# Kernel optimization log

Hardware: AMD Instinct MI355X
Metric: run time of the kernel (lower is better)

Reference implementation:

```python
import jax, jax.numpy as jnp
import numpy as np

B, C, H, W = 8, 3, 512, 512


def _spd(key, shape_prefix, c):
    a = jax.random.normal(key, shape_prefix + (c, c), dtype=jnp.float32)
    return a @ jnp.swapaxes(a, -1, -2) + jnp.eye(c, dtype=jnp.float32)


def setup_inputs() -> dict:
    key = jax.random.key(0)
    k1, k2, k3, k4, k5 = jax.random.split(key, 5)
    target = jax.random.normal(k1, (B, C, H, W), dtype=jnp.float32)
    mu = jax.random.normal(k2, (B, C, H, W), dtype=jnp.float32)
    # per-pixel covariance matrices; sigma_y must be SPD for inverse/log-det
    sigma_mu = _spd(k3, (B, H, W), C)
    sigma_n = _spd(k4, (B, H, W), C)
    sigma_y = _spd(k5, (B, H, W), C)
    return {"target": target, "mu": mu, "sigma_mu": sigma_mu,
            "sigma_n": sigma_n, "sigma_y": sigma_y}


def reference(target, mu, sigma_mu, sigma_n, sigma_y):
    # T: residual per pixel, channels-last  [B,H,W,C]
    T = jnp.transpose(target - mu, (0, 2, 3, 1))
    inv = jnp.linalg.inv(sigma_y)                      # [B,H,W,C,C] tiny 3x3 batched inverse
    # quadratic form 0.5 * T^t Sigma^{-1} T            [B,H,W]
    t1 = 0.5 * jnp.einsum('bhwc,bhwcd,bhwd->bhw', T, inv, T)
    t2 = 0.5 * jnp.log(jnp.linalg.det(sigma_y))        # [B,H,W]
    loss = jnp.mean(t1 + t2)
    # torch code zeroes loss if quadratic term blows up
    loss = jnp.where(jnp.max(t1) > 1e8, jnp.zeros_like(loss), loss)
    return loss
```

## Files before the change

### kernel.cpp

```cpp
#include <hip/hip_runtime.h>

constexpr int Cc = 3;
constexpr int Hc = 512;
constexpr int Wc = 512;
constexpr int HW = Hc * Wc;
constexpr int NPIX = 8 * HW;
constexpr int NGRP = NPIX / 4;
constexpr int NBLK = NGRP / 256;


__global__ __launch_bounds__(256) void map_loss_main(
    const float* __restrict__ target,
    const float* __restrict__ mu,
    const float* __restrict__ sigma_y,
    double* __restrict__ part_sum,
    float* __restrict__ part_max)
{
    double local_sum = 0.0;
    float local_max = 0.0f;

    int g = blockIdx.x * blockDim.x + threadIdx.x;
    {
        int p0 = g << 2;
        int b  = p0 >> 18;
        int hw = p0 & (HW - 1);
        long long base = (long long)b * (Cc * HW) + hw;

        const float4* tg = (const float4*)(target + base);
        const float4* mm = (const float4*)(mu + base);
        float4 d0 = tg[0];            float4 m0 = mm[0];
        float4 d1 = tg[HW / 4];       float4 m1 = mm[HW / 4];
        float4 d2 = tg[2 * HW / 4];   float4 m2 = mm[2 * HW / 4];
        d0.x -= m0.x; d0.y -= m0.y; d0.z -= m0.z; d0.w -= m0.w;
        d1.x -= m1.x; d1.y -= m1.y; d1.z -= m1.z; d1.w -= m1.w;
        d2.x -= m2.x; d2.y -= m2.y; d2.z -= m2.z; d2.w -= m2.w;

        union { float4 v[9]; float f[36]; } S;
        const float4* s4 = (const float4*)(sigma_y + (long long)p0 * 9);
        #pragma unroll
        for (int i = 0; i < 9; ++i) S.v[i] = s4[i];

        const float T0[4] = {d0.x, d0.y, d0.z, d0.w};
        const float T1[4] = {d1.x, d1.y, d1.z, d1.w};
        const float T2[4] = {d2.x, d2.y, d2.z, d2.w};

        #pragma unroll
        for (int i = 0; i < 4; ++i) {
            const float* s = S.f + i * 9;
            float s00 = s[0], s01 = s[1], s02 = s[2];
            float s11 = s[4], s12 = s[5], s22 = s[8];

            float a00 = s11 * s22 - s12 * s12;
            float a01 = s02 * s12 - s01 * s22;
            float a02 = s01 * s12 - s02 * s11;
            float a11 = s00 * s22 - s02 * s02;
            float a12 = s01 * s02 - s00 * s12;
            float a22 = s00 * s11 - s01 * s01;

            float det = s00 * a00 + s01 * a01 + s02 * a02;

            float t0 = T0[i], t1 = T1[i], t2 = T2[i];
            float quad = t0 * t0 * a00 + t1 * t1 * a11 + t2 * t2 * a22
                       + 2.0f * (t0 * t1 * a01 + t0 * t2 * a02 + t1 * t2 * a12);

            float t1term = 0.5f * quad / det;
            float t2term = 0.5f * logf(det);

            local_sum += (double)(t1term + t2term);
            local_max = fmaxf(local_max, t1term);
        }
    }

    for (int off = 32; off > 0; off >>= 1) {
        local_sum += __shfl_down(local_sum, off, 64);
        local_max = fmaxf(local_max, __shfl_down(local_max, off, 64));
    }

    __shared__ double ssum[4];
    __shared__ float  smax[4];
    int wave = threadIdx.x >> 6;
    int lane = threadIdx.x & 63;
    if (lane == 0) { ssum[wave] = local_sum; smax[wave] = local_max; }
    __syncthreads();

    if (threadIdx.x == 0) {
        part_sum[blockIdx.x] = ssum[0] + ssum[1] + ssum[2] + ssum[3];
        part_max[blockIdx.x] = fmaxf(fmaxf(smax[0], smax[1]), fmaxf(smax[2], smax[3]));
    }
}

__global__ __launch_bounds__(256) void map_loss_finalize(
    const double* __restrict__ part_sum,
    const float* __restrict__ part_max,
    float* __restrict__ out)
{
    double s = 0.0;
    float m = 0.0f;
    for (int i = threadIdx.x; i < NBLK; i += 256) {
        s += part_sum[i];
        m = fmaxf(m, part_max[i]);
    }

    for (int off = 32; off > 0; off >>= 1) {
        s += __shfl_down(s, off, 64);
        m = fmaxf(m, __shfl_down(m, off, 64));
    }

    __shared__ double ssum[4];
    __shared__ float  smax[4];
    int wave = threadIdx.x >> 6;
    int lane = threadIdx.x & 63;
    if (lane == 0) { ssum[wave] = s; smax[wave] = m; }
    __syncthreads();

    if (threadIdx.x == 0) {
        double bs = ssum[0] + ssum[1] + ssum[2] + ssum[3];
        float  bm = fmaxf(fmaxf(smax[0], smax[1]), fmaxf(smax[2], smax[3]));
        out[0] = (bm > 1e8f) ? 0.0f : (float)(bs / (double)NPIX);
    }
}

extern "C" void kernel_launch(void* const* d_in, const int* in_sizes, int n_in,
                              void* d_out, int out_size, void* d_ws, size_t ws_size,
                              hipStream_t stream) {
    const float* target  = (const float*)d_in[0];
    const float* mu      = (const float*)d_in[1];
    const float* sigma_y = (const float*)d_in[4];
    float* out = (float*)d_out;

    double* part_sum = (double*)d_ws;
    float*  part_max = (float*)((char*)d_ws + NBLK * sizeof(double));

    map_loss_main<<<NBLK, 256, 0, stream>>>(target, mu, sigma_y, part_sum, part_max);
    map_loss_finalize<<<1, 256, 0, stream>>>(part_sum, part_max, out);
}
```

Measured before the change: 218.3 us.

## Stage sigma_y through LDS with coalesced direct-to-LDS loads and XOR swizzle

The block's contiguous slab of sigma_y is now loaded cooperatively with global_load_lds, so each wave reads consecutive 16-byte chunks instead of each thread striding 144 bytes. Each thread then reads its own 9 float4s back from LDS, with an XOR swizzle on the index to reduce bank conflicts. This is meant to improve global-load coalescing on the dominant input stream. In exchange it adds 36KB of LDS per block and a barrier, and the launch bounds now request 4 blocks per CU.

```diff
diff --git a/kernel.cpp b/kernel.cpp
--- a/kernel.cpp
+++ b/kernel.cpp
@@ -5,70 +5,93 @@
 constexpr int Wc = 512;
 constexpr int HW = Hc * Wc;
 constexpr int NPIX = 8 * HW;
-constexpr int NGRP = NPIX / 4;
-constexpr int NBLK = NGRP / 256;
+constexpr int TPB  = 256;
+constexpr int PPT  = 4;
+constexpr int PPB  = TPB * PPT;
+constexpr int NBLK = NPIX / PPB;
+constexpr int SIG4_PER_BLK = PPB * 9 / 4;
 
 
-__global__ __launch_bounds__(256) void map_loss_main(
+__global__ __launch_bounds__(256, 4) void map_loss_main(
     const float* __restrict__ target,
     const float* __restrict__ mu,
     const float* __restrict__ sigma_y,
     double* __restrict__ part_sum,
     float* __restrict__ part_max)
 {
+    __shared__ float4 lds4[SIG4_PER_BLK];
+
+    const int tid = threadIdx.x;
+    const int bid = blockIdx.x;
+
+    const int g = bid * TPB + tid;
+    const long long p0 = (long long)g << 2;
+    const int b  = (int)(p0 >> 18);
+    const int hw = (int)p0 & (HW - 1);
+    const long long base = (long long)b * (Cc * HW) + hw;
+
+    const float4* tg = (const float4*)(target + base);
+    const float4* mm = (const float4*)(mu + base);
+    float4 d0 = tg[0];        float4 m0 = mm[0];
+    float4 d1 = tg[HW / 4];   float4 m1 = mm[HW / 4];
+    float4 d2 = tg[HW / 2];   float4 m2 = mm[HW / 2];
+
+    const float4* sblk = (const float4*)sigma_y + (long long)bid * SIG4_PER_BLK;
+    const int w = tid >> 6;
+    #pragma unroll
+    for (int j = 0; j < 9; ++j) {
+        const int s = j * TPB + tid;
+        const int c = (s >> 6) & 7;
+        __builtin_amdgcn_global_load_lds(
+            (const __attribute__((address_space(1))) void*)(sblk + (s ^ c)),
+            (__attribute__((address_space(3))) void*)(&lds4[j * TPB + w * 64]),
+            16, 0, 0);
+    }
+    __syncthreads();
+
+    d0.x -= m0.x; d0.y -= m0.y; d0.z -= m0.z; d0.w -= m0.w;
+    d1.x -= m1.x; d1.y -= m1.y; d1.z -= m1.z; d1.w -= m1.w;
+    d2.x -= m2.x; d2.y -= m2.y; d2.z -= m2.z; d2.w -= m2.w;
+
+    union { float4 v[9]; float f[36]; } S;
+    #pragma unroll
+    for (int k = 0; k < 9; ++k) {
+        const int r = 9 * tid + k;
+        const int x = r ^ ((r >> 6) & 7);
+        S.v[k] = lds4[x];
+    }
+
     double local_sum = 0.0;
     float local_max = 0.0f;
 
-    int g = blockIdx.x * blockDim.x + threadIdx.x;
-    {
-        int p0 = g << 2;
-        int b  = p0 >> 18;
-        int hw = p0 & (HW - 1);
-        long long base = (long long)b * (Cc * HW) + hw;
+    const float T0[4] = {d0.x, d0.y, d0.z, d0.w};
+    const float T1[4] = {d1.x, d1.y, d1.z, d1.w};
+    const float T2[4] = {d2.x, d2.y, d2.z, d2.w};
 
-        const float4* tg = (const float4*)(target + base);
-        const float4* mm = (const float4*)(mu + base);
-        float4 d0 = tg[0];            float4 m0 = mm[0];
-        float4 d1 = tg[HW / 4];       float4 m1 = mm[HW / 4];
-        float4 d2 = tg[2 * HW / 4];   float4 m2 = mm[2 * HW / 4];
-        d0.x -= m0.x; d0.y -= m0.y; d0.z -= m0.z; d0.w -= m0.w;
-        d1.x -= m1.x; d1.y -= m1.y; d1.z -= m1.z; d1.w -= m1.w;
-        d2.x -= m2.x; d2.y -= m2.y; d2.z -= m2.z; d2.w -= m2.w;
+    #pragma unroll
+    for (int i = 0; i < 4; ++i) {
+        const float* s = S.f + i * 9;
+        float s00 = s[0], s01 = s[1], s02 = s[2];
+        float s11 = s[4], s12 = s[5], s22 = s[8];
 
-        union { float4 v[9]; float f[36]; } S;
-        const float4* s4 = (const float4*)(sigma_y + (long long)p0 * 9);
-        #pragma unroll
-        for (int i = 0; i < 9; ++i) S.v[i] = s4[i];
+        float a00 = s11 * s22 - s12 * s12;
+        float a01 = s02 * s12 - s01 * s22;
+        float a02 = s01 * s12 - s02 * s11;
+        float a11 = s00 * s22 - s02 * s02;
+        float a12 = s01 * s02 - s00 * s12;
+        float a22 = s00 * s11 - s01 * s01;
 
-        const float T0[4] = {d0.x, d0.y, d0.z, d0.w};
-        const float T1[4] = {d1.x, d1.y, d1.z, d1.w};
-        const float T2[4] = {d2.x, d2.y, d2.z, d2.w};
+        float det = s00 * a00 + s01 * a01 + s02 * a02;
 
-        #pragma unroll
-        for (int i = 0; i < 4; ++i) {
-            const float* s = S.f + i * 9;
-            float s00 = s[0], s01 = s[1], s02 = s[2];
-            float s11 = s[4], s12 = s[5], s22 = s[8];
+        float t0 = T0[i], t1 = T1[i], t2 = T2[i];
+        float quad = t0 * t0 * a00 + t1 * t1 * a11 + t2 * t2 * a22
+                   + 2.0f * (t0 * t1 * a01 + t0 * t2 * a02 + t1 * t2 * a12);
 
-            float a00 = s11 * s22 - s12 * s12;
-            float a01 = s02 * s12 - s01 * s22;
-            float a02 = s01 * s12 - s02 * s11;
-            float a11 = s00 * s22 - s02 * s02;
-            float a12 = s01 * s02 - s00 * s12;
-            float a22 = s00 * s11 - s01 * s01;
+        float t1term = 0.5f * quad / det;
+        float t2term = 0.5f * logf(det);
 
-            float det = s00 * a00 + s01 * a01 + s02 * a02;
-
-            float t0 = T0[i], t1 = T1[i], t2 = T2[i];
-            float quad = t0 * t0 * a00 + t1 * t1 * a11 + t2 * t2 * a22
-                       + 2.0f * (t0 * t1 * a01 + t0 * t2 * a02 + t1 * t2 * a12);
-
-            float t1term = 0.5f * quad / det;
-            float t2term = 0.5f * logf(det);
-
-            local_sum += (double)(t1term + t2term);
-            local_max = fmaxf(local_max, t1term);
-        }
+        local_sum += (double)(t1term + t2term);
+        local_max = fmaxf(local_max, t1term);
     }
 
     for (int off = 32; off > 0; off >>= 1) {
@@ -78,9 +101,8 @@
 
     __shared__ double ssum[4];
     __shared__ float  smax[4];
-    int wave = threadIdx.x >> 6;
     int lane = threadIdx.x & 63;
-    if (lane == 0) { ssum[wave] = local_sum; smax[wave] = local_max; }
+    if (lane == 0) { ssum[w] = local_sum; smax[w] = local_max; }
     __syncthreads();
 
     if (threadIdx.x == 0) {
@@ -131,6 +153,6 @@
     double* part_sum = (double*)d_ws;
     float*  part_max = (float*)((char*)d_ws + NBLK * sizeof(double));
 
-    map_loss_main<<<NBLK, 256, 0, stream>>>(target, mu, sigma_y, part_sum, part_max);
+    map_loss_main<<<NBLK, TPB, 0, stream>>>(target, mu, sigma_y, part_sum, part_max);
     map_loss_finalize<<<1, 256, 0, stream>>>(part_sum, part_max, out);
 }
```

After: 215.3 us. No clear change (-1.4%).
